# Kernel optimization log

Measured on AMD Instinct MI355X. Metric: run time of the kernel, lower is better.

Reference implementation:

```python
import jax, jax.numpy as jnp
import numpy as np


def setup_inputs() -> dict:
    key = jax.random.key(0)
    k1, k2, k3 = jax.random.split(key, 3)
    x = jax.random.normal(k1, (32, 256, 32, 32), dtype=jnp.float32)
    weight = jax.random.normal(k2, (256, 256, 3, 3), dtype=jnp.float32) * 0.05
    bias = jax.random.normal(k3, (256,), dtype=jnp.float32) * 0.01
    return {"x": x, "weight": weight, "bias": bias}


def _forward(x, weight, bias):
    B, cin, n, _ = x.shape
    cout, _, k, _ = weight.shape
    s = (k - 1) // 2
    nf = n // 2 + 1
    bins = n * nf

    # fft shift matrix: exp(-1j*2*pi*s*(i+j)/n), kept rfft columns
    idx = jnp.arange(n)
    shift = idx[None, :] + idx[:, None]                     # (n, n)
    shift_m = jnp.exp(-1j * 2 * jnp.pi * s * shift / n)[:, :nf]
    shift_m = shift_m.reshape(bins, 1, 1).astype(jnp.complex64)

    # xfft: (B, cin, n, nf) -> (bins, cin, B)
    xfft = jnp.fft.rfft2(x)
    xfft = jnp.transpose(xfft, (2, 3, 1, 0)).reshape(bins, cin, B)

    # Hfft: (cout, cin, n, nf) -> (bins, cout, cin), shifted + conj
    Hfft = jnp.fft.rfft2(weight, s=(n, n)).reshape(cout, cin, bins)
    Hfft = shift_m * jnp.conj(jnp.transpose(Hfft, (2, 0, 1)))

    def sq_abs(z):
        return jnp.real(z) ** 2 + jnp.imag(z) ** 2

    RowNorm = jnp.sqrt(jnp.sum(sq_abs(Hfft), axis=2))       # (bins, cout)
    ColNorm = jnp.sqrt(jnp.sum(sq_abs(Hfft), axis=1))       # (bins, cin)

    if cout >= cin:
        RowLoss = jnp.mean((RowNorm - jnp.sqrt(cin / cout)) ** 2)
        ColLoss = jnp.mean((ColNorm - 1.0) ** 2)
        HHT = jnp.einsum('npc,nqc->npq', jnp.conj(Hfft), Hfft)  # (bins, cout, cout)
        mask = jnp.triu(jnp.ones((cout, cout), bool), k=1)
        count = bins * (cout * (cout - 1) // 2)
        AngLoss = jnp.sum(sq_abs(HHT) * mask[None]) / count   # MSE(|HHT[triu]|, 0)
        L = cout * ColLoss + cin * RowLoss + AngLoss
    else:
        RowLoss = jnp.mean((RowNorm - 1.0) ** 2)
        ColLoss = jnp.mean((ColNorm - jnp.sqrt(cout / cin)) ** 2)
        HTH = jnp.einsum('ndp,ndq->npq', jnp.conj(Hfft), Hfft)  # (bins, cin, cin)
        mask = jnp.triu(jnp.ones((cin, cin), bool), k=1)
        count = bins * (cin * (cin - 1) // 2)
        AngLoss = jnp.sum(sq_abs(HTH) * mask[None]) / count
        L = cout * ColLoss + cin * RowLoss + AngLoss

    # per-bin complex matmul: (bins, cout, cin) @ (bins, cin, B) -> (bins, cout, B)
    yfft = Hfft @ xfft
    yfft = jnp.transpose(yfft.reshape(n, nf, cout, B), (3, 2, 0, 1))  # (B, cout, n, nf)
    y = jnp.fft.irfft2(yfft, s=(n, n))
    y = y + bias[None, :, None, None]
    return y, L


def reference(x, weight, bias):
    return _forward(x, weight, bias)
```

## Files before the change

kernel.cpp:

```cpp
#include <hip/hip_runtime.h>
#include <math.h>

typedef __attribute__((ext_vector_type(8)))  short  short8;
typedef __attribute__((ext_vector_type(16))) float  float16;

#define TWO_PI_OVER_32 0.19634954084936207f

static __device__ __forceinline__ unsigned short f2bf(float f) {
    unsigned int u = __float_as_uint(f);
    u = (u + 0x7FFFu + ((u >> 16) & 1u)) >> 16;
    return (unsigned short)u;
}
static __device__ __forceinline__ float bf2f(unsigned short s) {
    return __uint_as_float(((unsigned int)s) << 16);
}

static __device__ __forceinline__ void g2l16(const void* g, void* l) {
    __builtin_amdgcn_global_load_lds(
        (const __attribute__((address_space(1))) unsigned int*)g,
        (__attribute__((address_space(3))) unsigned int*)l, 16, 0, 0);
}

__global__ __launch_bounds__(256) void k_prepx(const float* __restrict__ x,
                                               unsigned short* __restrict__ xb,
                                               const float* __restrict__ w,
                                               unsigned short* __restrict__ wt,
                                               unsigned short* __restrict__ Vb,
                                               float* __restrict__ Drow,
                                               float* __restrict__ Dcol) {
    int tid = threadIdx.x;
    if (blockIdx.x < 4096) {
        int g = blockIdx.x * 256 + tid;
        int c = g & 31, r = (g >> 5) & 31, cig = (g >> 10) & 31, b = g >> 15;
        const float* xp = x + ((b * 256 + cig * 8) * 32 + r) * 32 + c;
        union { unsigned short u[8]; uint4 v; } pk;
        #pragma unroll
        for (int u = 0; u < 8; ++u) pk.u[u] = f2bf(xp[u * 1024]);
        ((uint4*)xb)[g] = pk.v;
        return;
    }
    __shared__ float sdata[45];
    __shared__ float ws2[256 * 9];
    int blk = blockIdx.x - 4096, lane = tid & 63;
    bool colmode = blk >= 256;
    int pc = blk & 255;
    if (tid < 45) sdata[tid] = 0.f;

    int p = colmode ? tid : pc;
    int c = colmode ? pc : tid;
    float w9[9];
    #pragma unroll
    for (int t = 0; t < 9; ++t) w9[t] = w[(p * 256 + c) * 9 + t];
    if (!colmode) {
        #pragma unroll
        for (int t = 0; t < 9; ++t) ws2[tid * 9 + t] = w9[t];
    }
    __syncthreads();

    int idx = 0;
    for (int ta = 0; ta < 9; ++ta)
        for (int tb = ta; tb < 9; ++tb) {
            float v = w9[ta] * w9[tb];
            #pragma unroll
            for (int off = 32; off > 0; off >>= 1) v += __shfl_down(v, off);
            if (lane == 0) atomicAdd(&sdata[idx], v);
            ++idx;
        }
    __syncthreads();
    if (tid < 45) (colmode ? Dcol : Drow)[tid * 256 + pc] = sdata[tid];

    if (!colmode) {
        #pragma unroll
        for (int t = 0; t < 9; ++t)
            wt[t * 65536 + (c >> 3) * 2048 + p * 8 + (c & 7)] = f2bf(w9[t]);
        if (tid < 320) {
            int ta = tid >> 5, cig = tid & 31;
            union { unsigned short u[8]; uint4 v; } pk;
            #pragma unroll
            for (int u = 0; u < 8; ++u)
                pk.u[u] = (ta < 9) ? f2bf(ws2[(cig * 8 + u) * 9 + ta]) : (unsigned short)0;
            ((uint4*)Vb)[(p * 10 + ta) * 32 + cig] = pk.v;
        }
    }
}

#define XBUF 18432
#define WBUF 18432
#define BUFSTRIDE 36864

__global__ __launch_bounds__(256, 2) void k_conv(const unsigned short* __restrict__ xb,
                                                 const unsigned short* __restrict__ wt,
                                                 const float* __restrict__ bias,
                                                 const unsigned short* __restrict__ Vb,
                                                 unsigned short* __restrict__ Gb,
                                                 float* __restrict__ y) {
    extern __shared__ unsigned char smem[];

    const int tid  = threadIdx.x;
    const int lane = tid & 63;
    const int half = lane >> 5;
    const int m    = lane & 31;

    if (blockIdx.x >= 256) {
        int blk = blockIdx.x - 256, I = 0;
        while (blk >= 20 - I) { blk -= 20 - I; ++I; }
        int J = I + blk;
        const int wave = tid >> 6;
        const int wm = wave >> 1, wn = wave & 1;
        const int row0 = I * 128 + wm * 64;
        const int col0 = J * 128 + wn * 64;

        float16 acc[2][2];
        #pragma unroll
        for (int i = 0; i < 2; ++i)
            #pragma unroll
            for (int j = 0; j < 2; ++j)
                #pragma unroll
                for (int r = 0; r < 16; ++r) acc[i][j][r] = 0.f;

        const short8* vb = (const short8*)Vb;
        for (int kc = 0; kc < 16; ++kc) {
            int cig = kc * 2 + half;
            short8 a0 = vb[(row0 + m) * 32 + cig];
            short8 a1 = vb[(row0 + 32 + m) * 32 + cig];
            short8 b0 = vb[(col0 + m) * 32 + cig];
            short8 b1 = vb[(col0 + 32 + m) * 32 + cig];
            acc[0][0] = __builtin_amdgcn_mfma_f32_32x32x16_bf16(a0, b0, acc[0][0], 0, 0, 0);
            acc[0][1] = __builtin_amdgcn_mfma_f32_32x32x16_bf16(a0, b1, acc[0][1], 0, 0, 0);
            acc[1][0] = __builtin_amdgcn_mfma_f32_32x32x16_bf16(a1, b0, acc[1][0], 0, 0, 0);
            acc[1][1] = __builtin_amdgcn_mfma_f32_32x32x16_bf16(a1, b1, acc[1][1], 0, 0, 0);
        }
        #pragma unroll
        for (int i = 0; i < 2; ++i)
            #pragma unroll
            for (int j = 0; j < 2; ++j)
                #pragma unroll
                for (int reg = 0; reg < 16; ++reg) {
                    int crow = (reg & 3) + 8 * (reg >> 2) + 4 * half;
                    Gb[(row0 + i * 32 + crow) * 2560 + col0 + j * 32 + m] =
                        f2bf(acc[i][j][reg]);
                }
        return;
    }

    const int wv    = tid >> 6;
    const int id    = blockIdx.x;
    const int xcd   = id & 7;
    const int local = id >> 3;
    const int b     = xcd * 4 + (local >> 3);
    const int rem   = local & 7;
    const int co0   = (rem & 3) * 64;
    const int r0    = (rem >> 2) * 16;

    float16 acc[2][4];
    #pragma unroll
    for (int i = 0; i < 2; ++i)
        #pragma unroll
        for (int ns = 0; ns < 4; ++ns)
            #pragma unroll
            for (int r = 0; r < 16; ++r) acc[i][ns][r] = 0.f;

    const uint4* xbv = (const uint4*)xb;
    const uint4* wtv = (const uint4*)wt;

    const int cigl = lane >> 5;
    const int coll = lane & 31;

    auto stage = [&](int buf, int kc) {
        uint4* xd = (uint4*)(smem + buf * BUFSTRIDE);
        uint4* wd = (uint4*)(smem + buf * BUFSTRIDE + XBUF);
        #pragma unroll
        for (int ch = wv; ch < 36; ch += 4) {
            if (ch < 18) {
                int gr = (r0 + ch + 31) & 31;
                g2l16(&xbv[((b * 32 + kc * 2 + cigl) * 32 + gr) * 32 + coll],
                      &xd[ch * 64]);
            } else {
                int wc = ch - 18;
                int t = wc >> 1, cig = wc & 1;
                g2l16(&wtv[t * 8192 + (kc * 2 + cig) * 256 + co0 + lane],
                      &wd[wc * 64]);
            }
        }
    };

    auto compute = [&](int buf) {
        const short8* xsl = (const short8*)(smem + buf * BUFSTRIDE);
        const short8* wsl = (const short8*)(smem + buf * BUFSTRIDE + XBUF);
        #pragma unroll
        for (int btv = 0; btv < 3; ++btv) {
            short8 a0[3], a1[3];
            #pragma unroll
            for (int atv = 0; atv < 3; ++atv) {
                int t = atv * 3 + btv;
                a0[atv] = wsl[(t * 2 + half) * 64 + m];
                a1[atv] = wsl[(t * 2 + half) * 64 + 32 + m];
            }
            #pragma unroll
            for (int s = 0; s < 6; ++s) {
                short8 bf = xsl[((wv * 4 + s) * 2 + half) * 32 + ((m + btv + 31) & 31)];
                #pragma unroll
                for (int atv = 0; atv < 3; ++atv) {
                    int ns = s - atv;
                    if (ns >= 0 && ns < 4) {
                        acc[0][ns] = __builtin_amdgcn_mfma_f32_32x32x16_bf16(a0[atv], bf, acc[0][ns], 0, 0, 0);
                        acc[1][ns] = __builtin_amdgcn_mfma_f32_32x32x16_bf16(a1[atv], bf, acc[1][ns], 0, 0, 0);
                    }
                }
            }
        }
    };

    stage(0, 0);
    #pragma unroll 1
    for (int kc2 = 0; kc2 < 8; ++kc2) {
        __syncthreads();
        stage(1, 2 * kc2 + 1);
        compute(0);
        __syncthreads();
        if (kc2 < 7) stage(0, 2 * kc2 + 2);
        compute(1);
    }

    #pragma unroll
    for (int i = 0; i < 2; ++i) {
        #pragma unroll
        for (int ns = 0; ns < 4; ++ns) {
            int r = r0 + wv * 4 + ns;
            #pragma unroll
            for (int reg = 0; reg < 16; ++reg) {
                int crow = (reg & 3) + 8 * (reg >> 2) + 4 * half;
                int co = co0 + i * 32 + crow;
                y[(b * 256 + co) * 1024 + r * 32 + m] = acc[i][ns][reg] + bias[co];
            }
        }
    }
}

__global__ __launch_bounds__(256) void k_loss(const float* __restrict__ Drow,
                                              const float* __restrict__ Dcol,
                                              const unsigned short* __restrict__ Gb,
                                              float* __restrict__ rowp,
                                              float* __restrict__ colp,
                                              float* __restrict__ angp) {
    __shared__ union {
        struct { float coef[45]; float red[2]; } rc;
        struct { unsigned short gs[9 * 2560]; float red; } ang;
    } sh;
    int tid = threadIdx.x;

    if (blockIdx.x < 544) {
        int bin = blockIdx.x;
        int u = bin / 17, v = bin % 17;
        if (tid < 2) sh.rc.red[tid] = 0.f;
        if (tid < 45) {
            int idx = 0, TA = 0, TB = 0;
            for (int ta = 0; ta < 9; ++ta)
                for (int tb = ta; tb < 9; ++tb) {
                    if (idx == tid) { TA = ta; TB = tb; }
                    ++idx;
                }
            int da = TA / 3 - TB / 3;
            int db = TA % 3 - TB % 3;
            float cth = cosf(TWO_PI_OVER_32 * (float)(u * da + v * db));
            sh.rc.coef[tid] = (TA == TB) ? 1.f : 2.f * cth;
        }
        __syncthreads();

        float s1 = 0.f, s2 = 0.f;
        const float* dr = Drow + tid;
        const float* dc = Dcol + tid;
        #pragma unroll
        for (int i = 0; i < 45; ++i) {
            s1 += sh.rc.coef[i] * dr[i * 256];
            s2 += sh.rc.coef[i] * dc[i * 256];
        }
        float e1 = sqrtf(fmaxf(s1, 0.f)) - 1.f; e1 *= e1;
        float e2 = sqrtf(fmaxf(s2, 0.f)) - 1.f; e2 *= e2;
        #pragma unroll
        for (int off = 32; off > 0; off >>= 1) {
            e1 += __shfl_down(e1, off);
            e2 += __shfl_down(e2, off);
        }
        if ((tid & 63) == 0) { atomicAdd(&sh.rc.red[0], e1); atomicAdd(&sh.rc.red[1], e2); }
        __syncthreads();
        if (tid == 0) { rowp[bin] = sh.rc.red[0]; colp[bin] = sh.rc.red[1]; }
    } else {
        int p = blockIdx.x - 544;
        if (tid == 0) sh.ang.red = 0.f;
        uint4* gsv = (uint4*)sh.ang.gs;
        const uint4* gbv = (const uint4*)Gb;
        for (int i = tid; i < 2880; i += 256) {
            int rr = i / 320, cc = i - rr * 320;
            gsv[i] = gbv[(p * 10 + rr) * 320 + cc];
        }
        __syncthreads();

        int q = tid;
        float S = 0.f;
        if (q > p) {
            float g5[5][5];
            #pragma unroll
            for (int i = 0; i < 5; ++i)
                #pragma unroll
                for (int j = 0; j < 5; ++j) g5[i][j] = 0.f;
            #pragma unroll
            for (int ta = 0; ta < 9; ++ta)
                #pragma unroll
                for (int tb = 0; tb < 9; ++tb) {
                    float c = bf2f(sh.ang.gs[ta * 2560 + q * 10 + tb]);
                    g5[ta / 3 - tb / 3 + 2][ta % 3 - tb % 3 + 2] += c;
                }
            #pragma unroll
            for (int da = 0; da < 5; ++da) {
                const float* g = g5[da];
                float sq = g[0]*g[0] + g[1]*g[1] + g[2]*g[2] + g[3]*g[3] + g[4]*g[4];
                float cr = g[0]*g[2] + g[1]*g[3] + g[2]*g[4] + g[0]*g[4];
                S += 17.f * sq + 2.f * cr;
            }
            S *= 32.f;
        }
        #pragma unroll
        for (int off = 32; off > 0; off >>= 1) S += __shfl_down(S, off);
        if ((tid & 63) == 0) atomicAdd(&sh.ang.red, S);
        __syncthreads();
        if (tid == 0) angp[p] = sh.ang.red;
    }
}

__global__ __launch_bounds__(256) void k_fin(const float* __restrict__ rowp,
                                             const float* __restrict__ colp,
                                             const float* __restrict__ angp,
                                             float* __restrict__ out) {
    __shared__ float sred[3][4];
    int tid = threadIdx.x;
    float r = 0.f, c = 0.f, a = 0.f;
    for (int i = tid; i < 544; i += 256) { r += rowp[i]; c += colp[i]; }
    a = angp[tid];
    #pragma unroll
    for (int off = 32; off > 0; off >>= 1) {
        r += __shfl_down(r, off);
        c += __shfl_down(c, off);
        a += __shfl_down(a, off);
    }
    if ((tid & 63) == 0) {
        int wv = tid >> 6;
        sred[0][wv] = r; sred[1][wv] = c; sred[2][wv] = a;
    }
    __syncthreads();
    if (tid == 0) {
        float R = sred[0][0] + sred[0][1] + sred[0][2] + sred[0][3];
        float C = sred[1][0] + sred[1][1] + sred[1][2] + sred[1][3];
        float A = sred[2][0] + sred[2][1] + sred[2][2] + sred[2][3];
        out[8388608] = R / 544.f + C / 544.f + A / (544.f * 32640.f);
    }
}

extern "C" void kernel_launch(void* const* d_in, const int* in_sizes, int n_in,
                              void* d_out, int out_size, void* d_ws, size_t ws_size,
                              hipStream_t stream) {
    const float* x    = (const float*)d_in[0];
    const float* w    = (const float*)d_in[1];
    const float* bias = (const float*)d_in[2];
    float* out = (float*)d_out;

    char* ws = (char*)d_ws;
    unsigned short* wt = (unsigned short*)ws;
    unsigned short* xb = (unsigned short*)(ws + 1179648);
    unsigned short* Vb = (unsigned short*)(ws + 17956864);
    float* Drow  = (float*)(ws + 19267584);
    float* Dcol  = (float*)(ws + 19313664);
    float* rowp  = (float*)(ws + 19359744);
    float* colp  = (float*)(ws + 19361920);
    float* angp  = (float*)(ws + 19364096);
    unsigned short* Gb = (unsigned short*)(ws + 19392512);

    static bool smem_cfg = false;
    if (!smem_cfg) {
        hipFuncSetAttribute(reinterpret_cast<const void*>(k_conv),
                            hipFuncAttributeMaxDynamicSharedMemorySize, 73728);
        smem_cfg = true;
    }

    k_prepx <<<4608, 256, 0, stream>>>(x, xb, w, wt, Vb, Drow, Dcol);
    k_conv  <<<466, 256, 73728, stream>>>(xb, wt, bias, Vb, Gb, out);
    k_loss  <<<800, 256, 0, stream>>>(Drow, Dcol, Gb, rowp, colp, angp);
    k_fin   <<<1, 256, 0, stream>>>(rowp, colp, angp, out);
}
```

Baseline: 158.8 us.

## Halve conv row tile, use static LDS, and pipeline with explicit waitcnt barriers

The convolution tile is cut from 16 to 8 output rows per block, doubling the conv grid to 512 blocks and shrinking the LDS footprint so it fits in static shared memory. The double-buffered loop replaces __syncthreads with explicit vmcnt waits, raw s_barrier calls, and setprio around the MFMA phases, so the next stage's async loads stay in flight while the current buffer is computed. The aim is more parallelism across CUs and better overlap of loads with compute. In exchange, the 3x3 halo rows get reloaded more often relative to useful work and each block issues fewer MFMAs per weight load.

```diff
diff --git a/kernel.cpp b/kernel.cpp
--- a/kernel.cpp
+++ b/kernel.cpp
@@ -20,6 +20,11 @@
         (const __attribute__((address_space(1))) unsigned int*)g,
         (__attribute__((address_space(3))) unsigned int*)l, 16, 0, 0);
 }
+
+#define SBAR() do { __builtin_amdgcn_s_barrier(); \
+                    __builtin_amdgcn_sched_barrier(0); } while (0)
+#define WAITV(n) do { asm volatile("s_waitcnt vmcnt(" #n ")" ::: "memory"); \
+                      __builtin_amdgcn_sched_barrier(0); } while (0)
 
 __global__ __launch_bounds__(256) void k_prepx(const float* __restrict__ x,
                                                unsigned short* __restrict__ xb,
@@ -84,25 +89,22 @@
     }
 }
 
-#define XBUF 18432
-#define WBUF 18432
-#define BUFSTRIDE 36864
-
 __global__ __launch_bounds__(256, 2) void k_conv(const unsigned short* __restrict__ xb,
                                                  const unsigned short* __restrict__ wt,
                                                  const float* __restrict__ bias,
                                                  const unsigned short* __restrict__ Vb,
                                                  unsigned short* __restrict__ Gb,
                                                  float* __restrict__ y) {
-    extern __shared__ unsigned char smem[];
+    __shared__ unsigned short xs[2][640 * 8];
+    __shared__ unsigned short wsm[2][1152 * 8];
 
     const int tid  = threadIdx.x;
     const int lane = tid & 63;
     const int half = lane >> 5;
     const int m    = lane & 31;
 
-    if (blockIdx.x >= 256) {
-        int blk = blockIdx.x - 256, I = 0;
+    if (blockIdx.x >= 512) {
+        int blk = blockIdx.x - 512, I = 0;
         while (blk >= 20 - I) { blk -= 20 - I; ++I; }
         int J = I + blk;
         const int wave = tid >> 6;
@@ -147,16 +149,16 @@
     const int id    = blockIdx.x;
     const int xcd   = id & 7;
     const int local = id >> 3;
-    const int b     = xcd * 4 + (local >> 3);
-    const int rem   = local & 7;
+    const int b     = xcd * 4 + (local >> 4);
+    const int rem   = local & 15;
     const int co0   = (rem & 3) * 64;
-    const int r0    = (rem >> 2) * 16;
-
-    float16 acc[2][4];
+    const int r0    = (rem >> 2) * 8;
+
+    float16 acc[2][2];
     #pragma unroll
     for (int i = 0; i < 2; ++i)
         #pragma unroll
-        for (int ns = 0; ns < 4; ++ns)
+        for (int ns = 0; ns < 2; ++ns)
             #pragma unroll
             for (int r = 0; r < 16; ++r) acc[i][ns][r] = 0.f;
 
@@ -167,16 +169,16 @@
     const int coll = lane & 31;
 
     auto stage = [&](int buf, int kc) {
-        uint4* xd = (uint4*)(smem + buf * BUFSTRIDE);
-        uint4* wd = (uint4*)(smem + buf * BUFSTRIDE + XBUF);
-        #pragma unroll
-        for (int ch = wv; ch < 36; ch += 4) {
-            if (ch < 18) {
+        uint4* xd = (uint4*)xs[buf];
+        uint4* wd = (uint4*)wsm[buf];
+        #pragma unroll
+        for (int ch = wv; ch < 28; ch += 4) {
+            if (ch < 10) {
                 int gr = (r0 + ch + 31) & 31;
                 g2l16(&xbv[((b * 32 + kc * 2 + cigl) * 32 + gr) * 32 + coll],
                       &xd[ch * 64]);
             } else {
-                int wc = ch - 18;
+                int wc = ch - 10;
                 int t = wc >> 1, cig = wc & 1;
                 g2l16(&wtv[t * 8192 + (kc * 2 + cig) * 256 + co0 + lane],
                       &wd[wc * 64]);
@@ -185,8 +187,8 @@
     };
 
     auto compute = [&](int buf) {
-        const short8* xsl = (const short8*)(smem + buf * BUFSTRIDE);
-        const short8* wsl = (const short8*)(smem + buf * BUFSTRIDE + XBUF);
+        const short8* xsl = (const short8*)xs[buf];
+        const short8* wsl = (const short8*)wsm[buf];
         #pragma unroll
         for (int btv = 0; btv < 3; ++btv) {
             short8 a0[3], a1[3];
@@ -197,12 +199,12 @@
                 a1[atv] = wsl[(t * 2 + half) * 64 + 32 + m];
             }
             #pragma unroll
-            for (int s = 0; s < 6; ++s) {
-                short8 bf = xsl[((wv * 4 + s) * 2 + half) * 32 + ((m + btv + 31) & 31)];
+            for (int s = 0; s < 4; ++s) {
+                short8 bf = xsl[((wv * 2 + s) * 2 + half) * 32 + ((m + btv + 31) & 31)];
                 #pragma unroll
                 for (int atv = 0; atv < 3; ++atv) {
                     int ns = s - atv;
-                    if (ns >= 0 && ns < 4) {
+                    if (ns >= 0 && ns < 2) {
                         acc[0][ns] = __builtin_amdgcn_mfma_f32_32x32x16_bf16(a0[atv], bf, acc[0][ns], 0, 0, 0);
                         acc[1][ns] = __builtin_amdgcn_mfma_f32_32x32x16_bf16(a1[atv], bf, acc[1][ns], 0, 0, 0);
                     }
@@ -214,19 +216,26 @@
     stage(0, 0);
     #pragma unroll 1
     for (int kc2 = 0; kc2 < 8; ++kc2) {
-        __syncthreads();
         stage(1, 2 * kc2 + 1);
+        WAITV(7); SBAR();
+        __builtin_amdgcn_s_setprio(1);
         compute(0);
-        __syncthreads();
-        if (kc2 < 7) stage(0, 2 * kc2 + 2);
+        __builtin_amdgcn_s_setprio(0);
+        SBAR();
+        if (kc2 < 7) { stage(0, 2 * kc2 + 2); WAITV(7); }
+        else         { WAITV(0); }
+        SBAR();
+        __builtin_amdgcn_s_setprio(1);
         compute(1);
+        __builtin_amdgcn_s_setprio(0);
+        if (kc2 < 7) SBAR();
     }
 
     #pragma unroll
     for (int i = 0; i < 2; ++i) {
         #pragma unroll
-        for (int ns = 0; ns < 4; ++ns) {
-            int r = r0 + wv * 4 + ns;
+        for (int ns = 0; ns < 2; ++ns) {
+            int r = r0 + wv * 2 + ns;
             #pragma unroll
             for (int reg = 0; reg < 16; ++reg) {
                 int crow = (reg & 3) + 8 * (reg >> 2) + 4 * half;
@@ -375,15 +384,8 @@
     float* angp  = (float*)(ws + 19364096);
     unsigned short* Gb = (unsigned short*)(ws + 19392512);
 
-    static bool smem_cfg = false;
-    if (!smem_cfg) {
-        hipFuncSetAttribute(reinterpret_cast<const void*>(k_conv),
-                            hipFuncAttributeMaxDynamicSharedMemorySize, 73728);
-        smem_cfg = true;
-    }
-
     k_prepx <<<4608, 256, 0, stream>>>(x, xb, w, wt, Vb, Drow, Dcol);
-    k_conv  <<<466, 256, 73728, stream>>>(xb, wt, bias, Vb, Gb, out);
+    k_conv  <<<722, 256, 0, stream>>>(xb, wt, bias, Vb, Gb, out);
     k_loss  <<<800, 256, 0, stream>>>(Drow, Dcol, Gb, rowp, colp, angp);
     k_fin   <<<1, 256, 0, stream>>>(rowp, colp, angp, out);
 }
```

After: 156.2 us. No clear change (-1.7%).
